# Optimization experiments

Measured on AMD Instinct MI355X. Metric: run time of the kernel, lower is better.

## Reference

```python
import jax, jax.numpy as jnp
import numpy as np

EPS = 1e-5
LAM = 0.01  # sparsity_threshold (softshrink lambda)
NUM_BLOCKS = 8


def layer_norm(x, g, b):
    mu = jnp.mean(x, axis=-1, keepdims=True)
    var = jnp.mean(jnp.square(x - mu), axis=-1, keepdims=True)
    return (x - mu) * jax.lax.rsqrt(var + EPS) * g + b


def softshrink(v, lam):
    return jnp.where(jnp.abs(v) > lam, v - jnp.sign(v) * lam, jnp.zeros_like(v))


def afno_filter(x, w1, b1, w2, b2):
    # x: (B,H,W,C) real. Block-diagonal complex MLP in Fourier space.
    B, H, W, C = x.shape
    bs = C // NUM_BLOCKS
    xf = jnp.fft.rfft2(x, axes=(1, 2), norm="ortho")            # (B,H,W//2+1,C) complex
    xf = xf.reshape(B, H, W // 2 + 1, NUM_BLOCKS, bs)
    xr, xi = jnp.real(xf), jnp.imag(xf)
    # hard_thresholding_fraction = 1.0 with H==W -> all modes kept (slice is full array)
    o1r = jax.nn.relu(jnp.einsum('bhwni,nio->bhwno', xr, w1[0])
                      - jnp.einsum('bhwni,nio->bhwno', xi, w1[1]) + b1[0])
    o1i = jax.nn.relu(jnp.einsum('bhwni,nio->bhwno', xi, w1[0])
                      + jnp.einsum('bhwni,nio->bhwno', xr, w1[1]) + b1[1])
    o2r = (jnp.einsum('bhwni,nio->bhwno', o1r, w2[0])
           - jnp.einsum('bhwni,nio->bhwno', o1i, w2[1]) + b2[0])
    o2i = (jnp.einsum('bhwni,nio->bhwno', o1i, w2[0])
           + jnp.einsum('bhwni,nio->bhwno', o1r, w2[1]) + b2[1])
    o2r = softshrink(o2r, LAM)
    o2i = softshrink(o2i, LAM)
    yf = (o2r + 1j * o2i).reshape(B, H, W // 2 + 1, C)
    y = jnp.fft.irfft2(yf, s=(H, W), axes=(1, 2), norm="ortho")
    return y + x  # internal residual (bias) of AFNO2DLayer


def setup_inputs() -> dict:
    key = jax.random.key(0)
    ks = jax.random.split(key, 16)
    B, H, W, C = 2, 256, 256, 256
    bs = C // NUM_BLOCKS
    latent = 4 * C
    scale = 0.02
    return {
        "x": jax.random.normal(ks[0], (B, H, W, C), dtype=jnp.float32),
        "n1_g": jnp.ones((C,), jnp.float32),
        "n1_b": jnp.zeros((C,), jnp.float32),
        "n2_g": jnp.ones((C,), jnp.float32),
        "n2_b": jnp.zeros((C,), jnp.float32),
        "w1": scale * jax.random.normal(ks[1], (2, NUM_BLOCKS, bs, bs), jnp.float32),
        "b1": scale * jax.random.normal(ks[2], (2, NUM_BLOCKS, bs), jnp.float32),
        "w2": scale * jax.random.normal(ks[3], (2, NUM_BLOCKS, bs, bs), jnp.float32),
        "b2": scale * jax.random.normal(ks[4], (2, NUM_BLOCKS, bs), jnp.float32),
        "mw1": jax.random.normal(ks[5], (C, latent), jnp.float32) / np.sqrt(C),
        "mb1": jnp.zeros((latent,), jnp.float32),
        "mw2": jax.random.normal(ks[6], (latent, C), jnp.float32) / np.sqrt(latent),
        "mb2": jnp.zeros((C,), jnp.float32),
    }


def reference(x, n1_g, n1_b, n2_g, n2_b, w1, b1, w2, b2, mw1, mb1, mw2, mb2):
    residual = x
    h = layer_norm(x, n1_g, n1_b)
    h = afno_filter(h, w1, b1, w2, b2)
    # double_skip = True
    h = h + residual
    residual = h
    h = layer_norm(h, n2_g, n2_b)
    # MLP: Linear -> GELU (exact) -> Linear (drop = 0)
    h = jax.nn.gelu(h @ mw1 + mb1, approximate=False)
    h = h @ mw2 + mb2
    return h + residual
```

## Files before the change

kernel.cpp:

```cpp
#include <hip/hip_runtime.h>
#include <math.h>

#define CC 256
#define KF 129
#define NBK 8
#define BSZ 32
#define LAT 1024

typedef __attribute__((ext_vector_type(8))) __bf16 bf16x8;
typedef __attribute__((ext_vector_type(4))) float f32x4;
typedef __attribute__((ext_vector_type(4))) unsigned u32x4;

__device__ __forceinline__ float wred(float v){
#pragma unroll
  for (int o = 32; o; o >>= 1) v += __shfl_xor(v, o, 64);
  return v;
}

__device__ __forceinline__ unsigned short f2b(float f){
  unsigned u = __builtin_bit_cast(unsigned, f);
  unsigned r = u + 0x7fffu + ((u >> 16) & 1u);
  return (unsigned short)(r >> 16);
}
__device__ __forceinline__ float b2f(unsigned short h){
  unsigned u = ((unsigned)h) << 16;
  return __builtin_bit_cast(float, u);
}

__device__ __forceinline__ bf16x8 ldfrag(const unsigned short* p){
  return __builtin_bit_cast(bf16x8, *(const uint4*)p);
}
__device__ __forceinline__ bf16x8 negf(bf16x8 v){
  u32x4 u = __builtin_bit_cast(u32x4, v);
  u = u ^ 0x80008000u;
  return __builtin_bit_cast(bf16x8, u);
}

__device__ __forceinline__ float gelu_t(float v){
  float s = v * v;
  float t = v * fmaf(s, -0.0713575f, -1.5957691f);
  float e = __expf(t);
  return v * __builtin_amdgcn_rcpf(1.0f + e);
}

__device__ __forceinline__ void stage_ld(const unsigned short* __restrict__ gp,
    unsigned short* v, int sc, int w8){
#pragma unroll
  for (int j = 0; j < 8; ++j) v[j] = gp[(size_t)(w8 + j) * CC + sc];
}
__device__ __forceinline__ void stage_wr(const unsigned short* v,
    unsigned short* lds, int sc, int w8){
  uint4 u;
  u.x = (unsigned)v[0] | ((unsigned)v[1] << 16);
  u.y = (unsigned)v[2] | ((unsigned)v[3] << 16);
  u.z = (unsigned)v[4] | ((unsigned)v[5] << 16);
  u.w = (unsigned)v[6] | ((unsigned)v[7] << 16);
  *(uint4*)(lds + sc * 32 + 8 * ((w8 >> 3) ^ ((sc >> 1) & 3))) = u;
}

__device__ __forceinline__ bf16x8 bfrag(const unsigned short* lds, int g, int lr, int nf){
  int c = nf * 16 + lr;
  return ldfrag(lds + c * 32 + 8 * (g ^ ((c >> 1) & 3)));
}

__global__ __launch_bounds__(256) void k_init(const float* __restrict__ mw1,
    const float* __restrict__ mw2, const float* __restrict__ w1,
    const float* __restrict__ w2,
    unsigned short* __restrict__ Awr, unsigned short* __restrict__ Awi,
    unsigned short* __restrict__ Ahc, unsigned short* __restrict__ Ahs,
    unsigned short* __restrict__ Air, unsigned short* __restrict__ Aii,
    unsigned short* __restrict__ w1s, unsigned short* __restrict__ w2c,
    unsigned short* __restrict__ w1tr, unsigned short* __restrict__ w1ti,
    unsigned short* __restrict__ w2tr, unsigned short* __restrict__ w2ti){
  int i = blockIdx.x * 256 + threadIdx.x;
  if (i < 49152) {
    int m = i >> 8, w = i & 255;
    float t = (float)((m * w) & 255) / 128.0f;
    Awr[i] = f2b(cospif(t) * 0.0625f);
    Awi[i] = f2b(-sinpif(t) * 0.0625f);
  }
  if (i < 65536) {
    int k = i >> 8, h = i & 255;
    float t = (float)((k * h) & 255) / 128.0f;
    Ahc[i] = f2b(cospif(t) * 0.0625f);
    Ahs[i] = f2b(sinpif(t) * 0.0625f);
  }
  if (i < 32768) {
    int w = i >> 7, kw = i & 127;
    float t = (float)((kw * w) & 255) / 128.0f;
    float c = (kw == 0) ? 0.0625f : 0.125f;
    Air[i] = f2b(cospif(t) * c);
    Aii[i] = f2b(-sinpif(t) * c);
  }
  if (i < 8192) {
    int n = i >> 10, o = (i >> 5) & 31, ii = i & 31;
    int src = (n * BSZ + ii) * BSZ + o;
    w1tr[i] = f2b(w1[src]);
    w1ti[i] = f2b(w1[NBK * BSZ * BSZ + src]);
    w2tr[i] = f2b(w2[src]);
    w2ti[i] = f2b(w2[NBK * BSZ * BSZ + src]);
  }
  {
    int l = i >> 8, k2 = i & 255;
    w1s[(l << 8) | (k2 ^ ((l & 7) << 3))] = f2b(mw1[k2 * LAT + l]);
    int n = i >> 10, l2 = i & 1023;
    int ch = l2 >> 6, kk = l2 & 63;
    w2c[(size_t)((ch << 8) + n) * 64 + (kk ^ ((n & 7) << 3))] = f2b(mw2[l2 * CC + n]);
  }
}

__global__ __launch_bounds__(256) void k_ln1(const float* __restrict__ in,
    const float* __restrict__ g, const float* __restrict__ b,
    unsigned short* __restrict__ outb){
  int lane = threadIdx.x & 63;
  size_t row = (size_t)blockIdx.x * 4 + (threadIdx.x >> 6);
  float4 v = ((const float4*)(in + row * CC))[lane];
  float s = wred(v.x + v.y + v.z + v.w);
  float q = wred(v.x*v.x + v.y*v.y + v.z*v.z + v.w*v.w);
  float mean = s * (1.0f/CC);
  float rstd = rsqrtf(q * (1.0f/CC) - mean*mean + 1e-5f);
  float4 gv = ((const float4*)g)[lane];
  float4 bv = ((const float4*)b)[lane];
  ushort4 ob;
  ob.x = f2b((v.x - mean) * rstd * gv.x + bv.x);
  ob.y = f2b((v.y - mean) * rstd * gv.y + bv.y);
  ob.z = f2b((v.z - mean) * rstd * gv.z + bv.z);
  ob.w = f2b((v.w - mean) * rstd * gv.w + bv.w);
  ((ushort4*)(outb + row * CC))[lane] = ob;
}

__global__ __launch_bounds__(256) void k_gw(const unsigned short* __restrict__ h1b,
    const unsigned short* __restrict__ Awr, const unsigned short* __restrict__ Awi,
    unsigned short* __restrict__ Xr, unsigned short* __restrict__ Xi){
  __shared__ __align__(16) unsigned short sb[2][2048];
  int tid = threadIdx.x, wv = tid >> 6, lane = tid & 63, g = lane >> 4, lr = lane & 15;
  int sc = tid & 63, w8 = (tid >> 6) * 8;
  int bh = blockIdx.x, m0 = blockIdx.y * 64, n0 = blockIdx.z * 64;
  const unsigned short* Bsrc = h1b + (size_t)bh * 65536 + n0;
  int arow = m0 + wv * 16 + lr;
  f32x4 aR[4], aI[4];
#pragma unroll
  for (int i = 0; i < 4; ++i) { aR[i] = (f32x4){0,0,0,0}; aI[i] = (f32x4){0,0,0,0}; }
  unsigned short vb[8];
  stage_ld(Bsrc, vb, sc, w8);
  stage_wr(vb, sb[0], sc, w8);
  __syncthreads();
  for (int ks = 0; ks < 8; ++ks) {
    int cur = ks & 1;
    if (ks < 7) stage_ld(Bsrc + (size_t)(ks + 1) * 32 * CC, vb, sc, w8);
    bf16x8 ar = ldfrag(Awr + (size_t)arow * 256 + ks * 32 + g * 8);
    bf16x8 ai = ldfrag(Awi + (size_t)arow * 256 + ks * 32 + g * 8);
#pragma unroll
    for (int nf = 0; nf < 4; ++nf) {
      bf16x8 bf = bfrag(sb[cur], g, lr, nf);
      aR[nf] = __builtin_amdgcn_mfma_f32_16x16x32_bf16(ar, bf, aR[nf], 0, 0, 0);
      aI[nf] = __builtin_amdgcn_mfma_f32_16x16x32_bf16(ai, bf, aI[nf], 0, 0, 0);
    }
    if (ks < 7) {
      stage_wr(vb, sb[cur ^ 1], sc, w8);
      __syncthreads();
    }
  }
  int b = bh >> 8, h = bh & 255;
#pragma unroll
  for (int nf = 0; nf < 4; ++nf) {
    int c = n0 + nf * 16 + lr;
#pragma unroll
    for (int r = 0; r < 4; ++r) {
      int kw = m0 + wv * 16 + g * 4 + r;
      if (kw < KF) {
        size_t o = ((size_t)(b * KF + kw) * 256 + h) * 256 + c;
        Xr[o] = f2b(aR[nf][r]);
        Xi[o] = f2b(aI[nf][r]);
      }
    }
  }
}

template<int INV>
__global__ __launch_bounds__(256) void k_gh(const unsigned short* __restrict__ Bre,
    const unsigned short* __restrict__ Bim, const unsigned short* __restrict__ Ac,
    const unsigned short* __restrict__ As, unsigned short* __restrict__ Ore,
    unsigned short* __restrict__ Oim){
  __shared__ __align__(16) unsigned short sr[2][2048], si[2][2048];
  int tid = threadIdx.x, wv = tid >> 6, lane = tid & 63, g = lane >> 4, lr = lane & 15;
  int sc = tid & 63, w8 = (tid >> 6) * 8;
  int bkw = blockIdx.x, m0 = blockIdx.y * 128, n0 = blockIdx.z * 64;
  const unsigned short* srcR = Bre + (size_t)bkw * 65536 + n0;
  const unsigned short* srcI = Bim + (size_t)bkw * 65536 + n0;
  f32x4 accR[2][4], accI[2][4];
#pragma unroll
  for (int m = 0; m < 2; ++m)
#pragma unroll
    for (int i = 0; i < 4; ++i) { accR[m][i] = (f32x4){0,0,0,0}; accI[m][i] = (f32x4){0,0,0,0}; }
  unsigned short vr[8], vi[8];
  stage_ld(srcR, vr, sc, w8);
  stage_ld(srcI, vi, sc, w8);
  stage_wr(vr, sr[0], sc, w8);
  stage_wr(vi, si[0], sc, w8);
  __syncthreads();
  for (int ks = 0; ks < 8; ++ks) {
    int cur = ks & 1;
    if (ks < 7) {
      stage_ld(srcR + (size_t)(ks + 1) * 32 * CC, vr, sc, w8);
      stage_ld(srcI + (size_t)(ks + 1) * 32 * CC, vi, sc, w8);
    }
    bf16x8 bR[4], bI[4];
#pragma unroll
    for (int nf = 0; nf < 4; ++nf) { bR[nf] = bfrag(sr[cur], g, lr, nf); bI[nf] = bfrag(si[cur], g, lr, nf); }
#pragma unroll
    for (int mt = 0; mt < 2; ++mt) {
      int arow = m0 + mt * 64 + wv * 16 + lr;
      bf16x8 ac = ldfrag(Ac + (size_t)arow * 256 + ks * 32 + g * 8);
      bf16x8 as = ldfrag(As + (size_t)arow * 256 + ks * 32 + g * 8);
      bf16x8 asn = negf(as);
#pragma unroll
      for (int nf = 0; nf < 4; ++nf) {
        accR[mt][nf] = __builtin_amdgcn_mfma_f32_16x16x32_bf16(ac, bR[nf], accR[mt][nf], 0, 0, 0);
        accR[mt][nf] = __builtin_amdgcn_mfma_f32_16x16x32_bf16(INV ? asn : as, bI[nf], accR[mt][nf], 0, 0, 0);
        accI[mt][nf] = __builtin_amdgcn_mfma_f32_16x16x32_bf16(ac, bI[nf], accI[mt][nf], 0, 0, 0);
        accI[mt][nf] = __builtin_amdgcn_mfma_f32_16x16x32_bf16(INV ? as : asn, bR[nf], accI[mt][nf], 0, 0, 0);
      }
    }
    if (ks < 7) {
      stage_wr(vr, sr[cur ^ 1], sc, w8);
      stage_wr(vi, si[cur ^ 1], sc, w8);
      __syncthreads();
    }
  }
  if (!INV) {
#pragma unroll
    for (int mt = 0; mt < 2; ++mt)
#pragma unroll
      for (int nf = 0; nf < 4; ++nf) {
        int c = n0 + nf * 16 + lr;
#pragma unroll
        for (int r = 0; r < 4; ++r) {
          int kh = m0 + mt * 64 + wv * 16 + g * 4 + r;
          size_t o = ((size_t)bkw * 256 + kh) * 256 + c;
          Ore[o] = f2b(accR[mt][nf][r]);
          Oim[o] = f2b(accI[mt][nf][r]);
        }
      }
  } else {
    int b = (bkw >= KF) ? 1 : 0;
    int kw = bkw - b * KF;
#pragma unroll
    for (int mt = 0; mt < 2; ++mt)
#pragma unroll
      for (int nf = 0; nf < 4; ++nf) {
        int c = n0 + nf * 16 + lr;
#pragma unroll
        for (int r = 0; r < 4; ++r) {
          int h = m0 + mt * 64 + wv * 16 + g * 4 + r;
          size_t o = (((size_t)b * 256 + h) * KF + kw) * 256 + c;
          Ore[o] = f2b(accR[mt][nf][r]);
          Oim[o] = f2b(accI[mt][nf][r]);
        }
      }
  }
}

__global__ __launch_bounds__(256) void k_gwi(const unsigned short* __restrict__ Zr,
    const unsigned short* __restrict__ Zi, const unsigned short* __restrict__ Ar,
    const unsigned short* __restrict__ Ai, const float* __restrict__ x,
    const unsigned short* __restrict__ h1b, unsigned short* __restrict__ out1b){
  __shared__ __align__(16) unsigned short sr[2][2048], si[2][2048];
  int tid = threadIdx.x, wv = tid >> 6, lane = tid & 63, g = lane >> 4, lr = lane & 15;
  int sc = tid & 63, w8 = (tid >> 6) * 8;
  int bh = blockIdx.x, m0 = blockIdx.y * 128, n0 = blockIdx.z * 64;
  const unsigned short* srcR = Zr + (size_t)bh * 33024 + n0;
  const unsigned short* srcI = Zi + (size_t)bh * 33024 + n0;
  f32x4 acc[2][4];
#pragma unroll
  for (int m = 0; m < 2; ++m)
#pragma unroll
    for (int i = 0; i < 4; ++i) acc[m][i] = (f32x4){0,0,0,0};
  unsigned short vr[8], vi[8];
  stage_ld(srcR, vr, sc, w8);
  stage_ld(srcI, vi, sc, w8);
  stage_wr(vr, sr[0], sc, w8);
  stage_wr(vi, si[0], sc, w8);
  __syncthreads();
  for (int ks = 0; ks < 4; ++ks) {
    int cur = ks & 1;
    if (ks < 3) {
      stage_ld(srcR + (size_t)(ks + 1) * 32 * CC, vr, sc, w8);
      stage_ld(srcI + (size_t)(ks + 1) * 32 * CC, vi, sc, w8);
    }
    bf16x8 bR[4], bI[4];
#pragma unroll
    for (int nf = 0; nf < 4; ++nf) { bR[nf] = bfrag(sr[cur], g, lr, nf); bI[nf] = bfrag(si[cur], g, lr, nf); }
#pragma unroll
    for (int mt = 0; mt < 2; ++mt) {
      int arow = m0 + mt * 64 + wv * 16 + lr;
      bf16x8 ar = ldfrag(Ar + (size_t)arow * 128 + ks * 32 + g * 8);
      bf16x8 ai = ldfrag(Ai + (size_t)arow * 128 + ks * 32 + g * 8);
#pragma unroll
      for (int nf = 0; nf < 4; ++nf) {
        acc[mt][nf] = __builtin_amdgcn_mfma_f32_16x16x32_bf16(ar, bR[nf], acc[mt][nf], 0, 0, 0);
        acc[mt][nf] = __builtin_amdgcn_mfma_f32_16x16x32_bf16(ai, bI[nf], acc[mt][nf], 0, 0, 0);
      }
    }
    if (ks < 3) {
      stage_wr(vr, sr[cur ^ 1], sc, w8);
      stage_wr(vi, si[cur ^ 1], sc, w8);
      __syncthreads();
    }
  }
#pragma unroll
  for (int nf = 0; nf < 4; ++nf) {
    int c = n0 + nf * 16 + lr;
    float zn = b2f(Zr[(size_t)bh * 33024 + 32768 + c]) * 0.0625f;
#pragma unroll
    for (int mt = 0; mt < 2; ++mt)
#pragma unroll
      for (int r = 0; r < 4; ++r) {
        int w = m0 + mt * 64 + wv * 16 + g * 4 + r;
        size_t idx = ((size_t)bh * 256 + w) * 256 + c;
        float ny = (w & 1) ? -zn : zn;
        out1b[idx] = f2b(acc[mt][nf][r] + ny + b2f(h1b[idx]) + x[idx]);
      }
  }
}

__global__ __launch_bounds__(256) void k_bmlp(const unsigned short* __restrict__ Yr,
    const unsigned short* __restrict__ Yi,
    const unsigned short* __restrict__ w1tr, const unsigned short* __restrict__ w1ti,
    const unsigned short* __restrict__ w2tr, const unsigned short* __restrict__ w2ti,
    const float* __restrict__ b1, const float* __restrict__ b2,
    unsigned short* __restrict__ Or, unsigned short* __restrict__ Oi){
  __shared__ __align__(16) unsigned short mids[4][16][64];
  int tid = threadIdx.x;
  int wave = tid >> 6, lane = tid & 63;
  int g = lane >> 4, lr = lane & 15;
  size_t pos0 = (size_t)blockIdx.x * 64 + wave * 16;
  for (int n = 0; n < NBK; ++n) {
    bf16x8 axr = ldfrag(Yr + (pos0 + lr) * CC + n * BSZ + g * 8);
    bf16x8 axi = ldfrag(Yi + (pos0 + lr) * CC + n * BSZ + g * 8);
    f32x4 o1r[2], o1i[2];
#pragma unroll
    for (int nf = 0; nf < 2; ++nf) {
      bf16x8 bwr = ldfrag(w1tr + (n * BSZ + nf * 16 + lr) * BSZ + g * 8);
      bf16x8 bwi = ldfrag(w1ti + (n * BSZ + nf * 16 + lr) * BSZ + g * 8);
      f32x4 zr = (f32x4){0,0,0,0}, zi = (f32x4){0,0,0,0};
      zr = __builtin_amdgcn_mfma_f32_16x16x32_bf16(axr, bwr, zr, 0, 0, 0);
      zr = __builtin_amdgcn_mfma_f32_16x16x32_bf16(axi, negf(bwi), zr, 0, 0, 0);
      zi = __builtin_amdgcn_mfma_f32_16x16x32_bf16(axi, bwr, zi, 0, 0, 0);
      zi = __builtin_amdgcn_mfma_f32_16x16x32_bf16(axr, bwi, zi, 0, 0, 0);
      o1r[nf] = zr; o1i[nf] = zi;
    }
#pragma unroll
    for (int nf = 0; nf < 2; ++nf) {
      float br = b1[n * BSZ + nf * 16 + lr];
      float bi = b1[NBK * BSZ + n * BSZ + nf * 16 + lr];
#pragma unroll
      for (int r = 0; r < 4; ++r) {
        int row = g * 4 + r;
        int er = nf * 16 + lr;
        mids[wave][row][er ^ ((row & 7) << 3)] = f2b(fmaxf(o1r[nf][r] + br, 0.f));
        mids[wave][row][(32 + er) ^ ((row & 7) << 3)] = f2b(fmaxf(o1i[nf][r] + bi, 0.f));
      }
    }
    bf16x8 par = ldfrag(&mids[wave][lr][(g * 8) ^ ((lr & 7) << 3)]);
    bf16x8 pai = ldfrag(&mids[wave][lr][(32 + g * 8) ^ ((lr & 7) << 3)]);
#pragma unroll
    for (int nf = 0; nf < 2; ++nf) {
      bf16x8 bwr = ldfrag(w2tr + (n * BSZ + nf * 16 + lr) * BSZ + g * 8);
      bf16x8 bwi = ldfrag(w2ti + (n * BSZ + nf * 16 + lr) * BSZ + g * 8);
      f32x4 zr = (f32x4){0,0,0,0}, zi = (f32x4){0,0,0,0};
      zr = __builtin_amdgcn_mfma_f32_16x16x32_bf16(par, bwr, zr, 0, 0, 0);
      zr = __builtin_amdgcn_mfma_f32_16x16x32_bf16(pai, negf(bwi), zr, 0, 0, 0);
      zi = __builtin_amdgcn_mfma_f32_16x16x32_bf16(pai, bwr, zi, 0, 0, 0);
      zi = __builtin_amdgcn_mfma_f32_16x16x32_bf16(par, bwi, zi, 0, 0, 0);
      float cr = b2[n * BSZ + nf * 16 + lr];
      float ci = b2[NBK * BSZ + n * BSZ + nf * 16 + lr];
#pragma unroll
      for (int r = 0; r < 4; ++r) {
        float vr = zr[r] + cr, vi = zi[r] + ci;
        size_t idx = (pos0 + g * 4 + r) * CC + n * BSZ + nf * 16 + lr;
        Or[idx] = f2b((fabsf(vr) > 0.01f) ? (vr - copysignf(0.01f, vr)) : 0.f);
        Oi[idx] = f2b((fabsf(vi) > 0.01f) ? (vi - copysignf(0.01f, vi)) : 0.f);
      }
    }
  }
}

__global__ __launch_bounds__(256, 2) void k_mlp(const unsigned short* __restrict__ o1b,
    const float* __restrict__ n2g, const float* __restrict__ n2b,
    const unsigned short* __restrict__ w1s, const float* __restrict__ mb1,
    const unsigned short* __restrict__ w2c, const float* __restrict__ mb2,
    float* __restrict__ out){
  __shared__ __align__(16) unsigned short sw1[64 * 256];
  __shared__ __align__(16) unsigned short sw2[256 * 64];
  __shared__ __align__(16) unsigned short mids[64][64];
  int tid = threadIdx.x;
  int wave = tid >> 6, lane = tid & 63;
  int g = lane >> 4, lr = lane & 15;
  size_t row0 = (size_t)blockIdx.x * 64;
  bf16x8 areg[8];
  float s = 0.f, q = 0.f;
#pragma unroll
  for (int ks = 0; ks < 8; ++ks) {
    areg[ks] = ldfrag(o1b + (row0 + wave * 16 + lr) * CC + ks * 32 + g * 8);
    u32x4 u = __builtin_bit_cast(u32x4, areg[ks]);
#pragma unroll
    for (int j = 0; j < 4; ++j) {
      float lo = __builtin_bit_cast(float, u[j] << 16);
      float hi = __builtin_bit_cast(float, u[j] & 0xffff0000u);
      s += lo + hi;
      q += lo * lo + hi * hi;
    }
  }
  s += __shfl_xor(s, 16, 64); s += __shfl_xor(s, 32, 64);
  q += __shfl_xor(q, 16, 64); q += __shfl_xor(q, 32, 64);
  float mean = s * (1.0f / CC);
  float rstd = rsqrtf(q * (1.0f / CC) - mean * mean + 1e-5f);
#pragma unroll
  for (int ks = 0; ks < 8; ++ks) {
    u32x4 u = __builtin_bit_cast(u32x4, areg[ks]);
    u32x4 o;
#pragma unroll
    for (int j = 0; j < 4; ++j) {
      int c0 = ks * 32 + g * 8 + j * 2;
      float lo = __builtin_bit_cast(float, u[j] << 16);
      float hi = __builtin_bit_cast(float, u[j] & 0xffff0000u);
      float nlo = (lo - mean) * rstd * n2g[c0] + n2b[c0];
      float nhi = (hi - mean) * rstd * n2g[c0 + 1] + n2b[c0 + 1];
      o[j] = (unsigned)f2b(nlo) | ((unsigned)f2b(nhi) << 16);
    }
    areg[ks] = __builtin_bit_cast(bf16x8, o);
  }
  f32x4 acc2[4][4];
#pragma unroll
  for (int mi = 0; mi < 4; ++mi)
#pragma unroll
    for (int ni = 0; ni < 4; ++ni) acc2[mi][ni] = (f32x4){0.f, 0.f, 0.f, 0.f};
  for (int ch = 0; ch < 16; ++ch) {
    __syncthreads();
    {
      const uint4* s1 = (const uint4*)(w1s + (size_t)ch * 64 * 256);
      const uint4* s2 = (const uint4*)(w2c + (size_t)ch * 256 * 64);
      uint4* d1 = (uint4*)sw1;
      uint4* d2 = (uint4*)sw2;
#pragma unroll
      for (int it = 0; it < 8; ++it) d1[it * 256 + tid] = s1[it * 256 + tid];
#pragma unroll
      for (int it = 0; it < 8; ++it) d2[it * 256 + tid] = s2[it * 256 + tid];
    }
    __syncthreads();
    f32x4 acc1[4];
#pragma unroll
    for (int s2_ = 0; s2_ < 4; ++s2_) acc1[s2_] = (f32x4){0.f, 0.f, 0.f, 0.f};
#pragma unroll
    for (int ks = 0; ks < 8; ++ks) {
#pragma unroll
      for (int s2_ = 0; s2_ < 4; ++s2_) {
        int l = s2_ * 16 + lr;
        bf16x8 bf = ldfrag(sw1 + l * 256 + ((ks * 32 + g * 8) ^ ((lr & 7) << 3)));
        acc1[s2_] = __builtin_amdgcn_mfma_f32_16x16x32_bf16(areg[ks], bf, acc1[s2_], 0, 0, 0);
      }
    }
    int l0 = ch * 64;
#pragma unroll
    for (int s2_ = 0; s2_ < 4; ++s2_) {
      float bias = mb1[l0 + s2_ * 16 + lr];
#pragma unroll
      for (int r = 0; r < 4; ++r) {
        int row = wave * 16 + g * 4 + r;
        mids[row][(s2_ * 16 + lr) ^ ((row & 7) << 3)] = f2b(gelu_t(acc1[s2_][r] + bias));
      }
    }
    __syncthreads();
#pragma unroll
    for (int ks = 0; ks < 2; ++ks) {
      bf16x8 af[4], bfv[4];
#pragma unroll
      for (int mi = 0; mi < 4; ++mi)
        af[mi] = ldfrag(&mids[mi * 16 + lr][(ks * 32 + g * 8) ^ ((lr & 7) << 3)]);
#pragma unroll
      for (int ni = 0; ni < 4; ++ni)
        bfv[ni] = ldfrag(sw2 + (wave * 64 + ni * 16 + lr) * 64 + ((ks * 32 + g * 8) ^ ((lr & 7) << 3)));
#pragma unroll
      for (int mi = 0; mi < 4; ++mi)
#pragma unroll
        for (int ni = 0; ni < 4; ++ni)
          acc2[mi][ni] = __builtin_amdgcn_mfma_f32_16x16x32_bf16(af[mi], bfv[ni], acc2[mi][ni], 0, 0, 0);
    }
  }
#pragma unroll
  for (int mi = 0; mi < 4; ++mi)
#pragma unroll
    for (int ni = 0; ni < 4; ++ni) {
      int n = wave * 64 + ni * 16 + lr;
      float bias = mb2[n];
#pragma unroll
      for (int r = 0; r < 4; ++r) {
        size_t idx = (row0 + mi * 16 + g * 4 + r) * CC + n;
        out[idx] = acc2[mi][ni][r] + bias + b2f(o1b[idx]);
      }
    }
}

extern "C" void kernel_launch(void* const* d_in, const int* in_sizes, int n_in,
                              void* d_out, int out_size, void* d_ws, size_t ws_size,
                              hipStream_t stream) {
  const float* x   = (const float*)d_in[0];
  const float* n1g = (const float*)d_in[1];
  const float* n1b = (const float*)d_in[2];
  const float* n2g = (const float*)d_in[3];
  const float* n2b = (const float*)d_in[4];
  const float* w1  = (const float*)d_in[5];
  const float* b1  = (const float*)d_in[6];
  const float* w2  = (const float*)d_in[7];
  const float* b2  = (const float*)d_in[8];
  const float* mw1 = (const float*)d_in[9];
  const float* mb1 = (const float*)d_in[10];
  const float* mw2 = (const float*)d_in[11];
  const float* mb2 = (const float*)d_in[12];
  float* out = (float*)d_out;

  char* ws = (char*)d_ws;
  unsigned short* o1b = (unsigned short*)(ws);
  unsigned short* h1b = (unsigned short*)(ws + 134217728ull);
  unsigned short* Xr  = (unsigned short*)(ws + 201326592ull);
  unsigned short* Xi  = (unsigned short*)(ws + 235143168ull);
  unsigned short* Yr  = (unsigned short*)(ws + 268959744ull);
  unsigned short* Yi  = (unsigned short*)(ws + 302776320ull);
  unsigned short* Awr = (unsigned short*)(ws + 336592896ull);
  unsigned short* Awi = (unsigned short*)(ws + 336691200ull);
  unsigned short* Ahc = (unsigned short*)(ws + 336789504ull);
  unsigned short* Ahs = (unsigned short*)(ws + 336920576ull);
  unsigned short* Air = (unsigned short*)(ws + 337051648ull);
  unsigned short* Aii = (unsigned short*)(ws + 337117184ull);
  unsigned short* w1s = (unsigned short*)(ws + 337182720ull);
  unsigned short* w2c = (unsigned short*)(ws + 337707008ull);
  unsigned short* w1tr = (unsigned short*)(ws + 338231296ull);
  unsigned short* w1ti = (unsigned short*)(ws + 338247680ull);
  unsigned short* w2tr = (unsigned short*)(ws + 338264064ull);
  unsigned short* w2ti = (unsigned short*)(ws + 338280448ull);

  k_init<<<1024, 256, 0, stream>>>(mw1, mw2, w1, w2, Awr, Awi, Ahc, Ahs, Air, Aii,
                                   w1s, w2c, w1tr, w1ti, w2tr, w2ti);
  k_ln1<<<32768, 256, 0, stream>>>(x, n1g, n1b, h1b);
  k_gw<<<dim3(512, 3, 4), 256, 0, stream>>>(h1b, Awr, Awi, Xr, Xi);
  k_gh<0><<<dim3(258, 2, 4), 256, 0, stream>>>(Xr, Xi, Ahc, Ahs, Yr, Yi);
  k_bmlp<<<1032, 256, 0, stream>>>(Yr, Yi, w1tr, w1ti, w2tr, w2ti, b1, b2, Xr, Xi);
  k_gh<1><<<dim3(258, 2, 4), 256, 0, stream>>>(Xr, Xi, Ahc, Ahs, Yr, Yi);
  k_gwi<<<dim3(512, 2, 4), 256, 0, stream>>>(Yr, Yi, Air, Aii, x, h1b, o1b);
  k_mlp<<<2048, 256, 0, stream>>>(o1b, n2g, n2b, w1s, mb1, w2c, mb2, out);
}
```

Before: 630.3 us.

## Fuse block-diagonal complex MLP into forward H-axis DFT GEMM epilogue

```diff
diff --git a/kernel.cpp b/kernel.cpp
--- a/kernel.cpp
+++ b/kernel.cpp
@@ -177,12 +177,16 @@
   }
 }
 
-template<int INV>
-__global__ __launch_bounds__(256) void k_gh(const unsigned short* __restrict__ Bre,
+__global__ __launch_bounds__(256) void k_ghb(const unsigned short* __restrict__ Bre,
     const unsigned short* __restrict__ Bim, const unsigned short* __restrict__ Ac,
-    const unsigned short* __restrict__ As, unsigned short* __restrict__ Ore,
-    unsigned short* __restrict__ Oim){
+    const unsigned short* __restrict__ As,
+    const unsigned short* __restrict__ w1tr, const unsigned short* __restrict__ w1ti,
+    const unsigned short* __restrict__ w2tr, const unsigned short* __restrict__ w2ti,
+    const float* __restrict__ b1, const float* __restrict__ b2,
+    unsigned short* __restrict__ Ore, unsigned short* __restrict__ Oim){
   __shared__ __align__(16) unsigned short sr[2][2048], si[2][2048];
+  __shared__ __align__(16) unsigned short yrt[4][16][64], yit[4][16][64];
+  __shared__ __align__(16) unsigned short bmid[4][16][64];
   int tid = threadIdx.x, wv = tid >> 6, lane = tid & 63, g = lane >> 4, lr = lane & 15;
   int sc = tid & 63, w8 = (tid >> 6) * 8;
   int bkw = blockIdx.x, m0 = blockIdx.y * 128, n0 = blockIdx.z * 64;
@@ -217,9 +221,9 @@
 #pragma unroll
       for (int nf = 0; nf < 4; ++nf) {
         accR[mt][nf] = __builtin_amdgcn_mfma_f32_16x16x32_bf16(ac, bR[nf], accR[mt][nf], 0, 0, 0);
-        accR[mt][nf] = __builtin_amdgcn_mfma_f32_16x16x32_bf16(INV ? asn : as, bI[nf], accR[mt][nf], 0, 0, 0);
+        accR[mt][nf] = __builtin_amdgcn_mfma_f32_16x16x32_bf16(as, bI[nf], accR[mt][nf], 0, 0, 0);
         accI[mt][nf] = __builtin_amdgcn_mfma_f32_16x16x32_bf16(ac, bI[nf], accI[mt][nf], 0, 0, 0);
-        accI[mt][nf] = __builtin_amdgcn_mfma_f32_16x16x32_bf16(INV ? as : asn, bR[nf], accI[mt][nf], 0, 0, 0);
+        accI[mt][nf] = __builtin_amdgcn_mfma_f32_16x16x32_bf16(asn, bR[nf], accI[mt][nf], 0, 0, 0);
       }
     }
     if (ks < 7) {
@@ -228,37 +232,139 @@
       __syncthreads();
     }
   }
-  if (!INV) {
-#pragma unroll
-    for (int mt = 0; mt < 2; ++mt)
+#pragma unroll
+  for (int mt = 0; mt < 2; ++mt) {
+#pragma unroll
+    for (int nf = 0; nf < 4; ++nf) {
+#pragma unroll
+      for (int r = 0; r < 4; ++r) {
+        int p = g * 4 + r;
+        int e = nf * 16 + lr;
+        yrt[wv][p][e ^ ((p & 7) << 3)] = f2b(accR[mt][nf][r]);
+        yit[wv][p][e ^ ((p & 7) << 3)] = f2b(accI[mt][nf][r]);
+      }
+    }
+#pragma unroll
+    for (int cb = 0; cb < 2; ++cb) {
+      int n = (n0 >> 5) + cb;
+      bf16x8 axr = ldfrag(&yrt[wv][lr][(cb * 32 + g * 8) ^ ((lr & 7) << 3)]);
+      bf16x8 axi = ldfrag(&yit[wv][lr][(cb * 32 + g * 8) ^ ((lr & 7) << 3)]);
+      f32x4 o1r[2], o1i[2];
+#pragma unroll
+      for (int nf = 0; nf < 2; ++nf) {
+        bf16x8 bwr = ldfrag(w1tr + (n * BSZ + nf * 16 + lr) * BSZ + g * 8);
+        bf16x8 bwi = ldfrag(w1ti + (n * BSZ + nf * 16 + lr) * BSZ + g * 8);
+        f32x4 zr = (f32x4){0,0,0,0}, zi = (f32x4){0,0,0,0};
+        zr = __builtin_amdgcn_mfma_f32_16x16x32_bf16(axr, bwr, zr, 0, 0, 0);
+        zr = __builtin_amdgcn_mfma_f32_16x16x32_bf16(axi, negf(bwi), zr, 0, 0, 0);
+        zi = __builtin_amdgcn_mfma_f32_16x16x32_bf16(axi, bwr, zi, 0, 0, 0);
+        zi = __builtin_amdgcn_mfma_f32_16x16x32_bf16(axr, bwi, zi, 0, 0, 0);
+        o1r[nf] = zr; o1i[nf] = zi;
+      }
+#pragma unroll
+      for (int nf = 0; nf < 2; ++nf) {
+        float br = b1[n * BSZ + nf * 16 + lr];
+        float bi = b1[NBK * BSZ + n * BSZ + nf * 16 + lr];
+#pragma unroll
+        for (int r = 0; r < 4; ++r) {
+          int row = g * 4 + r;
+          int er = nf * 16 + lr;
+          bmid[wv][row][er ^ ((row & 7) << 3)] = f2b(fmaxf(o1r[nf][r] + br, 0.f));
+          bmid[wv][row][(32 + er) ^ ((row & 7) << 3)] = f2b(fmaxf(o1i[nf][r] + bi, 0.f));
+        }
+      }
+      bf16x8 par = ldfrag(&bmid[wv][lr][(g * 8) ^ ((lr & 7) << 3)]);
+      bf16x8 pai = ldfrag(&bmid[wv][lr][(32 + g * 8) ^ ((lr & 7) << 3)]);
+#pragma unroll
+      for (int nf = 0; nf < 2; ++nf) {
+        bf16x8 bwr = ldfrag(w2tr + (n * BSZ + nf * 16 + lr) * BSZ + g * 8);
+        bf16x8 bwi = ldfrag(w2ti + (n * BSZ + nf * 16 + lr) * BSZ + g * 8);
+        f32x4 zr = (f32x4){0,0,0,0}, zi = (f32x4){0,0,0,0};
+        zr = __builtin_amdgcn_mfma_f32_16x16x32_bf16(par, bwr, zr, 0, 0, 0);
+        zr = __builtin_amdgcn_mfma_f32_16x16x32_bf16(pai, negf(bwi), zr, 0, 0, 0);
+        zi = __builtin_amdgcn_mfma_f32_16x16x32_bf16(pai, bwr, zi, 0, 0, 0);
+        zi = __builtin_amdgcn_mfma_f32_16x16x32_bf16(par, bwi, zi, 0, 0, 0);
+        float cr = b2[n * BSZ + nf * 16 + lr];
+        float ci = b2[NBK * BSZ + n * BSZ + nf * 16 + lr];
+#pragma unroll
+        for (int r = 0; r < 4; ++r) {
+          float vr2 = zr[r] + cr, vi2 = zi[r] + ci;
+          int kh = m0 + mt * 64 + wv * 16 + g * 4 + r;
+          int c = n0 + cb * 32 + nf * 16 + lr;
+          size_t o = ((size_t)bkw * 256 + kh) * 256 + c;
+          Ore[o] = f2b((fabsf(vr2) > 0.01f) ? (vr2 - copysignf(0.01f, vr2)) : 0.f);
+          Oim[o] = f2b((fabsf(vi2) > 0.01f) ? (vi2 - copysignf(0.01f, vi2)) : 0.f);
+        }
+      }
+    }
+  }
+}
+
+__global__ __launch_bounds__(256) void k_ghi(const unsigned short* __restrict__ Bre,
+    const unsigned short* __restrict__ Bim, const unsigned short* __restrict__ Ac,
+    const unsigned short* __restrict__ As, unsigned short* __restrict__ Ore,
+    unsigned short* __restrict__ Oim){
+  __shared__ __align__(16) unsigned short sr[2][2048], si[2][2048];
+  int tid = threadIdx.x, wv = tid >> 6, lane = tid & 63, g = lane >> 4, lr = lane & 15;
+  int sc = tid & 63, w8 = (tid >> 6) * 8;
+  int bkw = blockIdx.x, m0 = blockIdx.y * 128, n0 = blockIdx.z * 64;
+  const unsigned short* srcR = Bre + (size_t)bkw * 65536 + n0;
+  const unsigned short* srcI = Bim + (size_t)bkw * 65536 + n0;
+  f32x4 accR[2][4], accI[2][4];
+#pragma unroll
+  for (int m = 0; m < 2; ++m)
+#pragma unroll
+    for (int i = 0; i < 4; ++i) { accR[m][i] = (f32x4){0,0,0,0}; accI[m][i] = (f32x4){0,0,0,0}; }
+  unsigned short vr[8], vi[8];
+  stage_ld(srcR, vr, sc, w8);
+  stage_ld(srcI, vi, sc, w8);
+  stage_wr(vr, sr[0], sc, w8);
+  stage_wr(vi, si[0], sc, w8);
+  __syncthreads();
+  for (int ks = 0; ks < 8; ++ks) {
+    int cur = ks & 1;
+    if (ks < 7) {
+      stage_ld(srcR + (size_t)(ks + 1) * 32 * CC, vr, sc, w8);
+      stage_ld(srcI + (size_t)(ks + 1) * 32 * CC, vi, sc, w8);
+    }
+    bf16x8 bR[4], bI[4];
+#pragma unroll
+    for (int nf = 0; nf < 4; ++nf) { bR[nf] = bfrag(sr[cur], g, lr, nf); bI[nf] = bfrag(si[cur], g, lr, nf); }
+#pragma unroll
+    for (int mt = 0; mt < 2; ++mt) {
+      int arow = m0 + mt * 64 + wv * 16 + lr;
+      bf16x8 ac = ldfrag(Ac + (size_t)arow * 256 + ks * 32 + g * 8);
+      bf16x8 as = ldfrag(As + (size_t)arow * 256 + ks * 32 + g * 8);
+      bf16x8 asn = negf(as);
 #pragma unroll
       for (int nf = 0; nf < 4; ++nf) {
-        int c = n0 + nf * 16 + lr;
-#pragma unroll
-        for (int r = 0; r < 4; ++r) {
-          int kh = m0 + mt * 64 + wv * 16 + g * 4 + r;
-          size_t o = ((size_t)bkw * 256 + kh) * 256 + c;
-          Ore[o] = f2b(accR[mt][nf][r]);
-          Oim[o] = f2b(accI[mt][nf][r]);
-        }
-      }
-  } else {
-    int b = (bkw >= KF) ? 1 : 0;
-    int kw = bkw - b * KF;
-#pragma unroll
-    for (int mt = 0; mt < 2; ++mt)
-#pragma unroll
-      for (int nf = 0; nf < 4; ++nf) {
-        int c = n0 + nf * 16 + lr;
-#pragma unroll
-        for (int r = 0; r < 4; ++r) {
-          int h = m0 + mt * 64 + wv * 16 + g * 4 + r;
-          size_t o = (((size_t)b * 256 + h) * KF + kw) * 256 + c;
-          Ore[o] = f2b(accR[mt][nf][r]);
-          Oim[o] = f2b(accI[mt][nf][r]);
-        }
-      }
-  }
+        accR[mt][nf] = __builtin_amdgcn_mfma_f32_16x16x32_bf16(ac, bR[nf], accR[mt][nf], 0, 0, 0);
+        accR[mt][nf] = __builtin_amdgcn_mfma_f32_16x16x32_bf16(asn, bI[nf], accR[mt][nf], 0, 0, 0);
+        accI[mt][nf] = __builtin_amdgcn_mfma_f32_16x16x32_bf16(ac, bI[nf], accI[mt][nf], 0, 0, 0);
+        accI[mt][nf] = __builtin_amdgcn_mfma_f32_16x16x32_bf16(as, bR[nf], accI[mt][nf], 0, 0, 0);
+      }
+    }
+    if (ks < 7) {
+      stage_wr(vr, sr[cur ^ 1], sc, w8);
+      stage_wr(vi, si[cur ^ 1], sc, w8);
+      __syncthreads();
+    }
+  }
+  int b = (bkw >= KF) ? 1 : 0;
+  int kw = bkw - b * KF;
+#pragma unroll
+  for (int mt = 0; mt < 2; ++mt)
+#pragma unroll
+    for (int nf = 0; nf < 4; ++nf) {
+      int c = n0 + nf * 16 + lr;
+#pragma unroll
+      for (int r = 0; r < 4; ++r) {
+        int h = m0 + mt * 64 + wv * 16 + g * 4 + r;
+        size_t o = (((size_t)b * 256 + h) * KF + kw) * 256 + c;
+        Ore[o] = f2b(accR[mt][nf][r]);
+        Oim[o] = f2b(accI[mt][nf][r]);
+      }
+    }
 }
 
 __global__ __launch_bounds__(256) void k_gwi(const unsigned short* __restrict__ Zr,
@@ -321,68 +427,6 @@
         float ny = (w & 1) ? -zn : zn;
         out1b[idx] = f2b(acc[mt][nf][r] + ny + b2f(h1b[idx]) + x[idx]);
       }
-  }
-}
-
-__global__ __launch_bounds__(256) void k_bmlp(const unsigned short* __restrict__ Yr,
-    const unsigned short* __restrict__ Yi,
-    const unsigned short* __restrict__ w1tr, const unsigned short* __restrict__ w1ti,
-    const unsigned short* __restrict__ w2tr, const unsigned short* __restrict__ w2ti,
-    const float* __restrict__ b1, const float* __restrict__ b2,
-    unsigned short* __restrict__ Or, unsigned short* __restrict__ Oi){
-  __shared__ __align__(16) unsigned short mids[4][16][64];
-  int tid = threadIdx.x;
-  int wave = tid >> 6, lane = tid & 63;
-  int g = lane >> 4, lr = lane & 15;
-  size_t pos0 = (size_t)blockIdx.x * 64 + wave * 16;
-  for (int n = 0; n < NBK; ++n) {
-    bf16x8 axr = ldfrag(Yr + (pos0 + lr) * CC + n * BSZ + g * 8);
-    bf16x8 axi = ldfrag(Yi + (pos0 + lr) * CC + n * BSZ + g * 8);
-    f32x4 o1r[2], o1i[2];
-#pragma unroll
-    for (int nf = 0; nf < 2; ++nf) {
-      bf16x8 bwr = ldfrag(w1tr + (n * BSZ + nf * 16 + lr) * BSZ + g * 8);
-      bf16x8 bwi = ldfrag(w1ti + (n * BSZ + nf * 16 + lr) * BSZ + g * 8);
-      f32x4 zr = (f32x4){0,0,0,0}, zi = (f32x4){0,0,0,0};
-      zr = __builtin_amdgcn_mfma_f32_16x16x32_bf16(axr, bwr, zr, 0, 0, 0);
-      zr = __builtin_amdgcn_mfma_f32_16x16x32_bf16(axi, negf(bwi), zr, 0, 0, 0);
-      zi = __builtin_amdgcn_mfma_f32_16x16x32_bf16(axi, bwr, zi, 0, 0, 0);
-      zi = __builtin_amdgcn_mfma_f32_16x16x32_bf16(axr, bwi, zi, 0, 0, 0);
-      o1r[nf] = zr; o1i[nf] = zi;
-    }
-#pragma unroll
-    for (int nf = 0; nf < 2; ++nf) {
-      float br = b1[n * BSZ + nf * 16 + lr];
-      float bi = b1[NBK * BSZ + n * BSZ + nf * 16 + lr];
-#pragma unroll
-      for (int r = 0; r < 4; ++r) {
-        int row = g * 4 + r;
-        int er = nf * 16 + lr;
-        mids[wave][row][er ^ ((row & 7) << 3)] = f2b(fmaxf(o1r[nf][r] + br, 0.f));
-        mids[wave][row][(32 + er) ^ ((row & 7) << 3)] = f2b(fmaxf(o1i[nf][r] + bi, 0.f));
-      }
-    }
-    bf16x8 par = ldfrag(&mids[wave][lr][(g * 8) ^ ((lr & 7) << 3)]);
-    bf16x8 pai = ldfrag(&mids[wave][lr][(32 + g * 8) ^ ((lr & 7) << 3)]);
-#pragma unroll
-    for (int nf = 0; nf < 2; ++nf) {
-      bf16x8 bwr = ldfrag(w2tr + (n * BSZ + nf * 16 + lr) * BSZ + g * 8);
-      bf16x8 bwi = ldfrag(w2ti + (n * BSZ + nf * 16 + lr) * BSZ + g * 8);
-      f32x4 zr = (f32x4){0,0,0,0}, zi = (f32x4){0,0,0,0};
-      zr = __builtin_amdgcn_mfma_f32_16x16x32_bf16(par, bwr, zr, 0, 0, 0);
-      zr = __builtin_amdgcn_mfma_f32_16x16x32_bf16(pai, negf(bwi), zr, 0, 0, 0);
-      zi = __builtin_amdgcn_mfma_f32_16x16x32_bf16(pai, bwr, zi, 0, 0, 0);
-      zi = __builtin_amdgcn_mfma_f32_16x16x32_bf16(par, bwi, zi, 0, 0, 0);
-      float cr = b2[n * BSZ + nf * 16 + lr];
-      float ci = b2[NBK * BSZ + n * BSZ + nf * 16 + lr];
-#pragma unroll
-      for (int r = 0; r < 4; ++r) {
-        float vr = zr[r] + cr, vi = zi[r] + ci;
-        size_t idx = (pos0 + g * 4 + r) * CC + n * BSZ + nf * 16 + lr;
-        Or[idx] = f2b((fabsf(vr) > 0.01f) ? (vr - copysignf(0.01f, vr)) : 0.f);
-        Oi[idx] = f2b((fabsf(vi) > 0.01f) ? (vi - copysignf(0.01f, vi)) : 0.f);
-      }
-    }
   }
 }
 
@@ -544,9 +588,9 @@
                                    w1s, w2c, w1tr, w1ti, w2tr, w2ti);
   k_ln1<<<32768, 256, 0, stream>>>(x, n1g, n1b, h1b);
   k_gw<<<dim3(512, 3, 4), 256, 0, stream>>>(h1b, Awr, Awi, Xr, Xi);
-  k_gh<0><<<dim3(258, 2, 4), 256, 0, stream>>>(Xr, Xi, Ahc, Ahs, Yr, Yi);
-  k_bmlp<<<1032, 256, 0, stream>>>(Yr, Yi, w1tr, w1ti, w2tr, w2ti, b1, b2, Xr, Xi);
-  k_gh<1><<<dim3(258, 2, 4), 256, 0, stream>>>(Xr, Xi, Ahc, Ahs, Yr, Yi);
-  k_gwi<<<dim3(512, 2, 4), 256, 0, stream>>>(Yr, Yi, Air, Aii, x, h1b, o1b);
+  k_ghb<<<dim3(258, 2, 4), 256, 0, stream>>>(Xr, Xi, Ahc, Ahs,
+                                             w1tr, w1ti, w2tr, w2ti, b1, b2, Yr, Yi);
+  k_ghi<<<dim3(258, 2, 4), 256, 0, stream>>>(Yr, Yi, Ahc, Ahs, Xr, Xi);
+  k_gwi<<<dim3(512, 2, 4), 256, 0, stream>>>(Xr, Xi, Air, Aii, x, h1b, o1b);
   k_mlp<<<2048, 256, 0, stream>>>(o1b, n2g, n2b, w1s, mb1, w2c, mb2, out);
 }
```

Result: no change. 619.4 us (-1.7%).
